# Kernel optimization log

Hardware: AMD Instinct MI355X
Metric: run time of the kernel (lower is better)

Reference implementation:

```python
import jax, jax.numpy as jnp
import numpy as np
from itertools import combinations

N_QUBITS = 8
N_TRASH = 2
N_LAYERS = 4
BATCH = 32768
DIM = 2 ** N_QUBITS  # 256


def _cz_pairs():
    # same CZ pattern as layer() in the torch module; all pairs are distinct,
    # and CZ gates are diagonal and commute, so they fuse into one sign mask.
    pairs = list(combinations(range(N_TRASH), 2))
    for idx in range(N_TRASH):
        for i in range(N_TRASH):
            for j in range(N_TRASH + i, N_QUBITS, N_TRASH):
                pairs.append(((idx + i) % N_TRASH, j))
    return pairs


def _cz_layer_sign():
    bits = np.indices((2,) * N_QUBITS)  # [n_qubits, 2,...,2]; wire 0 = MSB (PennyLane order)
    sign = np.ones((2,) * N_QUBITS, np.float32)
    for a, b in _cz_pairs():
        sign = sign * (1.0 - 2.0 * (bits[a] * bits[b]).astype(np.float32))
    return jnp.asarray(sign)[None]  # broadcast over batch

_CZ_SIGN = _cz_layer_sign()


def _ry(state, theta, w):
    # RY(theta) on wire w, batched over leading axis. state: [B,2,...,2] complex64
    c = jnp.cos(theta / 2).astype(jnp.complex64)
    s = jnp.sin(theta / 2).astype(jnp.complex64)
    g = jnp.stack([jnp.stack([c, -s]), jnp.stack([s, c])])  # [2,2]
    out = jnp.tensordot(g, state, axes=((1,), (1 + w,)))
    return jnp.moveaxis(out, 0, 1 + w)


def _axis_vec(vals, w):
    shape = [1] * (N_QUBITS + 1)
    shape[1 + w] = 2
    return jnp.asarray(vals, dtype=jnp.complex64).reshape(shape)


def _apply_pauli(state, w, p):
    if p == 'X':
        return jnp.flip(state, axis=1 + w)
    if p == 'Y':
        return jnp.flip(state, axis=1 + w) * _axis_vec([-1j, 1j], w)
    return state * _axis_vec([1.0 + 0j, -1.0 + 0j], w)  # Z


def _forward(x, weights):
    # AmplitudeEmbedding(normalize=True)
    norm = jnp.sqrt(jnp.sum(x * x, axis=-1, keepdims=True))
    psi = (x / norm).astype(jnp.complex64).reshape((-1,) + (2,) * N_QUBITS)
    for l in range(N_LAYERS - 1):
        for q in range(N_QUBITS):
            psi = _ry(psi, weights[l * N_QUBITS + q], q)
        psi = psi * _CZ_SIGN  # all CZs of the layer fused into one diagonal
    base = (N_LAYERS - 1) * N_QUBITS
    for q in range(N_TRASH):  # last_layer: RY on trash qubits only
        psi = _ry(psi, weights[base + q], q)

    axes = tuple(range(1, N_QUBITS + 1))
    conj_psi = jnp.conj(psi)

    def ev(op_state):
        return jnp.sum(conj_psi * op_state, axis=axes).real.astype(jnp.float32)

    w0, w1 = 6, 7
    terms = [
        ev(_apply_pauli(psi, w0, 'X')),
        ev(_apply_pauli(psi, w0, 'Y')),
        ev(_apply_pauli(psi, w0, 'Z')),
        ev(_apply_pauli(psi, w1, 'X')),
        ev(_apply_pauli(psi, w1, 'Y')),
        ev(_apply_pauli(psi, w1, 'Z')),
        ev(_apply_pauli(_apply_pauli(psi, w0, 'X'), w1, 'X')),
        ev(_apply_pauli(_apply_pauli(psi, w0, 'Y'), w1, 'Y')),
        ev(_apply_pauli(_apply_pauli(psi, w0, 'Z'), w1, 'Z')),
    ]
    return jnp.stack(terms, axis=1)  # [B, 9]


def setup_inputs() -> dict:
    key = jax.random.key(0)
    kx, kw = jax.random.split(key)
    x = jax.random.normal(kx, (BATCH, DIM), dtype=jnp.float32)
    n_w = N_LAYERS * N_QUBITS - (N_QUBITS - N_TRASH)  # 26
    weights = jax.random.normal(kw, (n_w,), dtype=jnp.float32)
    return {'x': x, 'weights': weights}


def reference(x, weights):
    return _forward(x, weights)
```

## Files before the change

kernel.cpp:

```cpp
#include <hip/hip_runtime.h>
#include <math.h>

#define DIM 256
typedef float v2f  __attribute__((ext_vector_type(2)));
typedef _Float16 f16x8 __attribute__((ext_vector_type(8)));
typedef _Float16 f16x4 __attribute__((ext_vector_type(4)));
typedef float f32x4 __attribute__((ext_vector_type(4)));

__device__ __forceinline__ v2f mk2(float a, float b) { v2f r; r.x = a; r.y = b; return r; }
__device__ __forceinline__ float rl(float v, int l) {
    return __uint_as_float(__builtin_amdgcn_readlane(__float_as_uint(v), l));
}

template<int B2>
__device__ __forceinline__ void ry_pk(v2f* v, float c, float s) {
#pragma unroll
    for (int p = 0; p < 16; ++p)
        if (!(p & (1 << B2))) {
            const int q = p | (1 << B2);
            v2f lo = v[p], hi = v[q];
            v[p] = c * lo - s * hi;
            v[q] = s * lo + c * hi;
        }
}
__device__ __forceinline__ void ry_intra(v2f* v, float c, float s) {
#pragma unroll
    for (int p = 0; p < 16; ++p) {
        float lo = v[p].x, hi = v[p].y;
        v[p].x = fmaf(-s, hi, c * lo);
        v[p].y = fmaf(s, lo, c * hi);
    }
}

__global__ __launch_bounds__(256) void qae_buildU(const float* __restrict__ w,
                                                  _Float16* __restrict__ uf) {
    __shared__ float4 lds4[2048];
    const int lane = threadIdx.x & 63;
    const int wid  = threadIdx.x >> 6;
    const int wave = blockIdx.x * 4 + wid;
    const int l3   = lane & 7;
    const int e    = lane >> 3;
    const int col  = wave * 8 + e;
    float4* W = lds4 + wid * 512 + e * 64;

    float h = 0.f;
    if (lane < 20) h = 0.5f * w[lane < 18 ? lane : lane + 4];
    const float cv = __cosf(h), sv = __sinf(h);
#define RYP(B2, slot) ry_pk<B2>(v, rl(cv, slot), rl(sv, slot))
#define RYI(slot)     ry_intra(v, rl(cv, slot), rl(sv, slot))

    const int a0 = (l3 >> 2) & 1, a1 = (l3 >> 1) & 1, a2 = l3 & 1;
    const int aa = a0 & a1, dd = a0 ^ a1;
    const float fE = (aa ^ (dd & a2)) ? -1.f : 1.f;
    const float fO = ((aa ^ (dd & a2)) ^ dd) ? -1.f : 1.f;
    const float pB = (__popc(l3) & 1) ? -1.f : 1.f;
    const v2f mA0 = mk2(fE, fO), mA1 = mk2(fO, fE);
    const v2f mBp = mk2(pB, -pB);

    v2f v[16];
#pragma unroll
    for (int p = 0; p < 16; ++p) v[p] = mk2(0.f, 0.f);
    if (((col >> 2) & 7) == l3) {
        const int p = 2 * (col >> 5) + ((col >> 1) & 1);
        if (col & 1) v[p].y = 1.f; else v[p].x = 1.f;
    }

    RYP(3, 0); RYP(2, 1); RYP(1, 2);
#pragma unroll
    for (int g = 0; g < 8; ++g)
        W[g * 8 + (l3 ^ g)] = make_float4(v[2*g].x, v[2*g].y, v[2*g+1].x, v[2*g+1].y);
#pragma unroll
    for (int k = 0; k < 8; ++k) {
        float4 f = W[l3 * 8 + (k ^ l3)];
        v[2*k] = mk2(f.x, f.y); v[2*k+1] = mk2(f.z, f.w);
    }
    RYP(3, 3); RYP(2, 4); RYP(1, 5); RYP(0, 6); RYI(7);
#pragma unroll
    for (int p = 0; p < 16; ++p) v[p] *= (__popc(p) & 1) ? mA1 : mA0;
    RYP(3, 11); RYP(2, 12); RYP(1, 13); RYP(0, 14); RYI(15);
#pragma unroll
    for (int k = 0; k < 8; ++k)
        W[l3 * 8 + (k ^ l3)] = make_float4(v[2*k].x, v[2*k].y, v[2*k+1].x, v[2*k+1].y);
#pragma unroll
    for (int g = 0; g < 8; ++g) {
        float4 f = W[g * 8 + (l3 ^ g)];
        v[2*g] = mk2(f.x, f.y); v[2*g+1] = mk2(f.z, f.w);
    }
    RYP(3, 8); RYP(2, 9); RYP(1, 10);
#pragma unroll
    for (int p = 0; p < 16; ++p) {
        const int b0 = (p >> 3) & 1, b1 = (p >> 2) & 1;
        if (b0 & b1)      v[p] = -v[p];
        else if (b0 ^ b1) v[p] *= (__popc(p & 3) & 1) ? -mBp : mBp;
    }
    RYP(3, 16); RYP(2, 17); RYP(0, 18); RYI(19);
#pragma unroll
    for (int p = 0; p < 16; ++p) {
        const int b0 = (p >> 3) & 1, b1 = (p >> 2) & 1;
        if (b0 & b1)      v[p] = -v[p];
        else if (b0 ^ b1) v[p] *= (__popc(p & 3) & 1) ? -mBp : mBp;
    }
#undef RYP
#undef RYI

    _Float16* T = (_Float16*)(lds4 + wid * 512);
#pragma unroll
    for (int p = 0; p < 16; ++p) {
        const int m0 = ((p >> 1) << 5) | (l3 << 2) | ((p & 1) << 1);
        T[m0 * 8 + e]       = (_Float16)v[p].x;
        T[(m0 + 1) * 8 + e] = (_Float16)v[p].y;
    }
    const int ksv = wave >> 2, lfh = (wave & 3) << 4;
#pragma unroll
    for (int i = 0; i < 4; ++i) {
        const int m = lane * 4 + i;
        const int mt = m >> 4, lf = (m & 15) | lfh;
        f16x8 t = *(const f16x8*)(T + m * 8);
        *(f16x8*)(uf + (size_t)(((mt * 8 + ksv) * 64 + lf) * 8)) = t;
    }
}

__global__ __launch_bounds__(256, 2) void qae_gemm(const float* __restrict__ x,
                                                   const _Float16* __restrict__ uf,
                                                   float* __restrict__ out, int batch) {
    __shared__ __align__(16) _Float16 Xs[4][4096];
    __shared__ __align__(16) _Float16 Ut[16384];
    const int lane  = threadIdx.x & 63;
    const int wid   = threadIdx.x >> 6;
    const int strip = blockIdx.x * 4 + wid;
    const int bl = lane & 15, bq = lane >> 4;
    const int b  = strip * 16 + bl;

    _Float16* Xw = Xs[wid];
#pragma unroll
    for (int r = 0; r < 16; ++r) {
        int gr = strip * 16 + r; if (gr >= batch) gr = batch - 1;
        const float4 f = *(const float4*)(x + (size_t)gr * DIM + lane * 4);
        f16x4 hh;
        hh[0] = (_Float16)f.x; hh[1] = (_Float16)f.y;
        hh[2] = (_Float16)f.z; hh[3] = (_Float16)f.w;
        *(f16x4*)(Xw + r * 256 + lane * 4) = hh;
    }
    f16x8 bf[8];
    float nrm = 0.f;
#pragma unroll
    for (int ks = 0; ks < 8; ++ks) {
        bf[ks] = *(const f16x8*)(Xw + bl * 256 + ks * 32 + bq * 8);
#pragma unroll
        for (int j = 0; j < 8; ++j) { float t = (float)bf[ks][j]; nrm = fmaf(t, t, nrm); }
    }

    float pX6 = 0, pX7 = 0, pXX = 0, pYY = 0, pZ6 = 0, pZ7 = 0, pZZ = 0;

#pragma unroll
    for (int ph = 0; ph < 4; ++ph) {
        __syncthreads();
        const float4* src = (const float4*)uf + (size_t)ph * 2048 + threadIdx.x;
        float4* dst = (float4*)Ut;
#pragma unroll
        for (int i = 0; i < 8; ++i)
            dst[i * 256 + threadIdx.x] = src[i * 256];
        __syncthreads();
#pragma unroll
        for (int mtl = 0; mtl < 4; ++mtl) {
            f32x4 acc = {0.f, 0.f, 0.f, 0.f};
#pragma unroll
            for (int ks = 0; ks < 8; ++ks) {
                f16x8 af = *(const f16x8*)(Ut + ((mtl * 8 + ks) * 64 + lane) * 8);
                acc = __builtin_amdgcn_mfma_f32_16x16x32_f16(af, bf[ks], acc, 0, 0, 0);
            }
            const float q0 = acc[0], q1 = acc[1], q2 = acc[2], q3 = acc[3];
            pX6 += q0 * q2 + q1 * q3;
            pX7 += q0 * q1 + q2 * q3;
            pXX += q0 * q3 + q1 * q2;
            pYY += q1 * q2 - q0 * q3;
            const float s0 = q0*q0, s1 = q1*q1, s2 = q2*q2, s3 = q3*q3;
            pZ6 += (s0 + s1) - (s2 + s3);
            pZ7 += (s0 - s1) + (s2 - s3);
            pZZ += (s0 - s1) - (s2 - s3);
        }
    }

#pragma unroll
    for (int m = 16; m <= 32; m <<= 1) {
        nrm += __shfl_xor(nrm, m);
        pX6 += __shfl_xor(pX6, m); pX7 += __shfl_xor(pX7, m);
        pXX += __shfl_xor(pXX, m); pYY += __shfl_xor(pYY, m);
        pZ6 += __shfl_xor(pZ6, m); pZ7 += __shfl_xor(pZ7, m);
        pZZ += __shfl_xor(pZZ, m);
    }

    if (b < batch && bq == 0) {
        const float inv = 1.f / nrm;
        float* o = out + (size_t)b * 9;
        o[0] = 2.f * pX6 * inv;  o[1] = 0.f;  o[2] = pZ6 * inv;
        o[3] = 2.f * pX7 * inv;  o[4] = 0.f;  o[5] = pZ7 * inv;
        o[6] = 2.f * pXX * inv;  o[7] = 2.f * pYY * inv;  o[8] = pZZ * inv;
    }
}

extern "C" void kernel_launch(void* const* d_in, const int* in_sizes, int n_in,
                              void* d_out, int out_size, void* d_ws, size_t ws_size,
                              hipStream_t stream) {
    const float* x = (const float*)d_in[0];
    const float* w = (const float*)d_in[1];
    float* out = (float*)d_out;
    _Float16* uf = (_Float16*)d_ws;
    const int batch = in_sizes[0] / DIM;

    qae_buildU<<<8, 256, 0, stream>>>(w, uf);

    const int strips = (batch + 15) / 16;
    qae_gemm<<<(strips + 3) / 4, 256, 0, stream>>>(x, uf, out, batch);
}
```

Measured before the change: 85.60 us.

## Keep U fragments in registers with persistent blocks splitting M across waves

The GEMM kernel becomes persistent (up to 512 blocks looping over 16-row strips). Each wave holds a quarter of the U matrix permanently in registers instead of reloading all of U through LDS for every block. The four waves share one staged X strip (padded rows, double-buffered index), write partial expectation values to LDS, and a cross-wave reduction combines them with the row norms. This removes the repeated global/LDS traffic for U but uses 128 VGPRs of fragments per thread and adds three block barriers per strip, with each strip computed by only one block.

```diff
diff --git a/kernel.cpp b/kernel.cpp
--- a/kernel.cpp
+++ b/kernel.cpp
@@ -122,80 +122,103 @@
 
 __global__ __launch_bounds__(256, 2) void qae_gemm(const float* __restrict__ x,
                                                    const _Float16* __restrict__ uf,
-                                                   float* __restrict__ out, int batch) {
-    __shared__ __align__(16) _Float16 Xs[4][4096];
-    __shared__ __align__(16) _Float16 Ut[16384];
-    const int lane  = threadIdx.x & 63;
-    const int wid   = threadIdx.x >> 6;
-    const int strip = blockIdx.x * 4 + wid;
-    const int bl = lane & 15, bq = lane >> 4;
-    const int b  = strip * 16 + bl;
-
-    _Float16* Xw = Xs[wid];
-#pragma unroll
-    for (int r = 0; r < 16; ++r) {
+                                                   float* __restrict__ out,
+                                                   int batch, int strips) {
+    __shared__ __align__(16) _Float16 Xs[2][16 * 264];
+    __shared__ __align__(16) float Nb[2][16][20];
+    __shared__ __align__(16) float Ps[4][16][8];
+    const int tid  = threadIdx.x;
+    const int lane = tid & 63, wid = tid >> 6;
+    const int bl   = lane & 15, bq = lane >> 4;
+    const int r    = tid >> 4,  q  = tid & 15;
+
+    f16x8 af[4][8];
+#pragma unroll
+    for (int mtl = 0; mtl < 4; ++mtl)
+#pragma unroll
+        for (int ks = 0; ks < 8; ++ks)
+            af[mtl][ks] = *(const f16x8*)(uf +
+                (size_t)((((wid * 4 + mtl) * 8 + ks) * 64 + lane) * 8));
+
+    int p = 0;
+    for (int strip = blockIdx.x; strip < strips; strip += gridDim.x) {
+        __syncthreads();
         int gr = strip * 16 + r; if (gr >= batch) gr = batch - 1;
-        const float4 f = *(const float4*)(x + (size_t)gr * DIM + lane * 4);
-        f16x4 hh;
-        hh[0] = (_Float16)f.x; hh[1] = (_Float16)f.y;
-        hh[2] = (_Float16)f.z; hh[3] = (_Float16)f.w;
-        *(f16x4*)(Xw + r * 256 + lane * 4) = hh;
-    }
-    f16x8 bf[8];
-    float nrm = 0.f;
-#pragma unroll
-    for (int ks = 0; ks < 8; ++ks) {
-        bf[ks] = *(const f16x8*)(Xw + bl * 256 + ks * 32 + bq * 8);
-#pragma unroll
-        for (int j = 0; j < 8; ++j) { float t = (float)bf[ks][j]; nrm = fmaf(t, t, nrm); }
-    }
-
-    float pX6 = 0, pX7 = 0, pXX = 0, pYY = 0, pZ6 = 0, pZ7 = 0, pZZ = 0;
-
-#pragma unroll
-    for (int ph = 0; ph < 4; ++ph) {
+        const float* xr = x + (size_t)gr * DIM;
+        float ns = 0.f;
+#pragma unroll
+        for (int i = 0; i < 4; ++i) {
+            const int c = q + i * 16;
+            const float4 f = *(const float4*)(xr + c * 4);
+            ns += f.x*f.x + f.y*f.y + f.z*f.z + f.w*f.w;
+            f16x4 hh;
+            hh[0] = (_Float16)f.x; hh[1] = (_Float16)f.y;
+            hh[2] = (_Float16)f.z; hh[3] = (_Float16)f.w;
+            *(f16x4*)(Xs[p] + r * 264 + c * 4) = hh;
+        }
+        Nb[p][r][q] = ns;
         __syncthreads();
-        const float4* src = (const float4*)uf + (size_t)ph * 2048 + threadIdx.x;
-        float4* dst = (float4*)Ut;
-#pragma unroll
-        for (int i = 0; i < 8; ++i)
-            dst[i * 256 + threadIdx.x] = src[i * 256];
-        __syncthreads();
+
+        f16x8 bf[8];
+#pragma unroll
+        for (int ks = 0; ks < 8; ++ks)
+            bf[ks] = *(const f16x8*)(Xs[p] + bl * 264 + ks * 32 + bq * 8);
+
+        float pX6 = 0, pX7 = 0, pXX = 0, pYY = 0, pZ6 = 0, pZ7 = 0, pZZ = 0;
 #pragma unroll
         for (int mtl = 0; mtl < 4; ++mtl) {
             f32x4 acc = {0.f, 0.f, 0.f, 0.f};
 #pragma unroll
-            for (int ks = 0; ks < 8; ++ks) {
-                f16x8 af = *(const f16x8*)(Ut + ((mtl * 8 + ks) * 64 + lane) * 8);
-                acc = __builtin_amdgcn_mfma_f32_16x16x32_f16(af, bf[ks], acc, 0, 0, 0);
-            }
+            for (int ks = 0; ks < 8; ++ks)
+                acc = __builtin_amdgcn_mfma_f32_16x16x32_f16(af[mtl][ks], bf[ks],
+                                                             acc, 0, 0, 0);
             const float q0 = acc[0], q1 = acc[1], q2 = acc[2], q3 = acc[3];
-            pX6 += q0 * q2 + q1 * q3;
-            pX7 += q0 * q1 + q2 * q3;
-            pXX += q0 * q3 + q1 * q2;
-            pYY += q1 * q2 - q0 * q3;
+            pX6 += q0*q2 + q1*q3;  pX7 += q0*q1 + q2*q3;
+            pXX += q0*q3 + q1*q2;  pYY += q1*q2 - q0*q3;
             const float s0 = q0*q0, s1 = q1*q1, s2 = q2*q2, s3 = q3*q3;
             pZ6 += (s0 + s1) - (s2 + s3);
             pZ7 += (s0 - s1) + (s2 - s3);
             pZZ += (s0 - s1) - (s2 - s3);
         }
-    }
-
-#pragma unroll
-    for (int m = 16; m <= 32; m <<= 1) {
-        nrm += __shfl_xor(nrm, m);
-        pX6 += __shfl_xor(pX6, m); pX7 += __shfl_xor(pX7, m);
-        pXX += __shfl_xor(pXX, m); pYY += __shfl_xor(pYY, m);
-        pZ6 += __shfl_xor(pZ6, m); pZ7 += __shfl_xor(pZ7, m);
-        pZZ += __shfl_xor(pZZ, m);
-    }
-
-    if (b < batch && bq == 0) {
-        const float inv = 1.f / nrm;
-        float* o = out + (size_t)b * 9;
-        o[0] = 2.f * pX6 * inv;  o[1] = 0.f;  o[2] = pZ6 * inv;
-        o[3] = 2.f * pX7 * inv;  o[4] = 0.f;  o[5] = pZ7 * inv;
-        o[6] = 2.f * pXX * inv;  o[7] = 2.f * pYY * inv;  o[8] = pZZ * inv;
+#pragma unroll
+        for (int m = 16; m <= 32; m <<= 1) {
+            pX6 += __shfl_xor(pX6, m); pX7 += __shfl_xor(pX7, m);
+            pXX += __shfl_xor(pXX, m); pYY += __shfl_xor(pYY, m);
+            pZ6 += __shfl_xor(pZ6, m); pZ7 += __shfl_xor(pZ7, m);
+            pZZ += __shfl_xor(pZZ, m);
+        }
+        if (bq == 0) {
+            float* ps = Ps[wid][bl];
+            ps[0] = pX6; ps[1] = pX7; ps[2] = pXX; ps[3] = pYY;
+            ps[4] = pZ6; ps[5] = pZ7; ps[6] = pZZ;
+        }
+        __syncthreads();
+
+        {
+            const int col = lane >> 2, wq = lane & 3;
+            const float4 pa = *(const float4*)&Ps[wq][col][0];
+            const float4 pb = *(const float4*)&Ps[wq][col][4];
+            const float4 nn = *(const float4*)&Nb[p][col][wq * 4];
+            float aX6 = pa.x, aX7 = pa.y, aXX = pa.z, aYY = pa.w;
+            float aZ6 = pb.x, aZ7 = pb.y, aZZ = pb.z;
+            float an  = nn.x + nn.y + nn.z + nn.w;
+#pragma unroll
+            for (int m = 1; m <= 2; m <<= 1) {
+                aX6 += __shfl_xor(aX6, m); aX7 += __shfl_xor(aX7, m);
+                aXX += __shfl_xor(aXX, m); aYY += __shfl_xor(aYY, m);
+                aZ6 += __shfl_xor(aZ6, m); aZ7 += __shfl_xor(aZ7, m);
+                aZZ += __shfl_xor(aZZ, m); an  += __shfl_xor(an, m);
+            }
+            const int ob = strip * 16 + col;
+            if (wq == 0 && ob < batch) {
+                const float inv = 1.f / an;
+                float* o = out + (size_t)ob * 9;
+                o[0] = 2.f * aX6 * inv;  o[1] = 0.f;  o[2] = aZ6 * inv;
+                o[3] = 2.f * aX7 * inv;  o[4] = 0.f;  o[5] = aZ7 * inv;
+                o[6] = 2.f * aXX * inv;  o[7] = 2.f * aYY * inv;  o[8] = aZZ * inv;
+            }
+        }
+        p ^= 1;
     }
 }
 
@@ -211,5 +234,6 @@
     qae_buildU<<<8, 256, 0, stream>>>(w, uf);
 
     const int strips = (batch + 15) / 16;
-    qae_gemm<<<(strips + 3) / 4, 256, 0, stream>>>(x, uf, out, batch);
-}
+    int blocks = 512; if (blocks > strips) blocks = strips;
+    qae_gemm<<<blocks, 256, 0, stream>>>(x, uf, out, batch, strips);
+}
```

After: 86.37 us. No clear change (+0.9%).
